# Kernel optimization log

Measured on AMD Instinct MI355X. Metric: run time of the kernel, lower is better.

Reference implementation:

```python
import jax, jax.numpy as jnp
import numpy as np

B, S, DIM, SECL = 32, 2048, 1024, 16  # dim = 2*hidden_dim


def setup_inputs() -> dict:
    key = jax.random.key(0)
    ks = jax.random.split(key, 10)
    return {
        "dec_hidden": jax.random.normal(ks[0], (B, DIM), jnp.float32),
        "enc_output": jax.random.normal(ks[1], (B, S, DIM), jnp.float32),
        "enc_feature": jax.random.normal(ks[2], (B, S, DIM), jnp.float32),
        "enc_mask": jnp.ones((B, S), jnp.float32),
        "sec_attn": jax.random.uniform(ks[3], (B, SECL), jnp.float32),
        "coverage": jax.random.uniform(ks[4], (B, S), jnp.float32),
        "W_dec": jax.random.normal(ks[5], (DIM, DIM), jnp.float32) * (1.0 / np.sqrt(DIM)),
        "b_dec": jax.random.normal(ks[6], (DIM,), jnp.float32) * 0.01,
        "v": jax.random.normal(ks[7], (DIM,), jnp.float32) * (1.0 / np.sqrt(DIM)),
        "w_cov": jax.random.normal(ks[8], (DIM,), jnp.float32) * 0.1,
    }


def reference(dec_hidden, enc_output, enc_feature, enc_mask, sec_attn, coverage,
              W_dec, b_dec, v, w_cov):
    # dec_feature: [B, dim], broadcast over src_len
    dec_feature = dec_hidden @ W_dec.T + b_dec
    # att_features = enc_feature + dec_feature + coverage * w_cov  -> [B, S, dim]
    att = enc_feature + dec_feature[:, None, :] + coverage[:, :, None] * w_cov[None, None, :]
    # scalar score per position: v . tanh(att)  -> [B, S]
    score = jnp.einsum('bsd,d->bs', jnp.tanh(att), v)
    # NOTE: the original multiplies sec_attn*score into attn_dist but immediately
    # overwrites it with softmax(score)*mask, so sec_attn does not affect outputs.
    attn = jax.nn.softmax(score, axis=1) * enc_mask
    attn = attn / jnp.sum(attn, axis=1, keepdims=True)
    # context = attn @ enc_output  -> [B, dim]
    context = jnp.einsum('bs,bsd->bd', attn, enc_output)
    coverage_new = coverage + attn
    return context, attn, coverage_new
```

## Files before the change

### kernel.cpp

```cpp
#include <hip/hip_runtime.h>

#define BB 32
#define SS 2048
#define DD 1024

typedef float f32x4 __attribute__((ext_vector_type(4)));

#if defined(__has_builtin)
#  if __has_builtin(__builtin_amdgcn_exp2f)
#    define EXP2F(x) __builtin_amdgcn_exp2f(x)
#  endif
#  if __has_builtin(__builtin_amdgcn_rcpf)
#    define RCPF(x) __builtin_amdgcn_rcpf(x)
#  endif
#endif
#ifndef EXP2F
#  define EXP2F(x) exp2f(x)
#endif
#ifndef RCPF
#  define RCPF(x) (1.0f / (x))
#endif

#define LOG2E 1.44269504088896340736f

__device__ __forceinline__ float fast_tanh(float x) {
    x = fminf(fmaxf(x, -20.0f), 20.0f);
    float e = EXP2F(x * (2.0f * LOG2E));
    return (e - 1.0f) * RCPF(e + 1.0f);
}

__device__ __forceinline__ f32x4 ntload4(const float* p) {
    return __builtin_nontemporal_load((const f32x4*)p);
}

__global__ __launch_bounds__(256) void k_decfeat(
    const float* __restrict__ dh, const float* __restrict__ W,
    const float* __restrict__ bd, float* __restrict__ df) {
    int wave = threadIdx.x >> 6, lane = threadIdx.x & 63;
    int i = blockIdx.x * 4 + wave;
    f32x4 w[4];
#pragma unroll
    for (int r = 0; r < 4; ++r)
        w[r] = ntload4(W + (size_t)i * DD + (lane + 64 * r) * 4);
    float bi = bd[i];
    for (int b = 0; b < BB; ++b) {
        const float* drow = dh + (size_t)b * DD;
        float acc = 0.0f;
#pragma unroll
        for (int r = 0; r < 4; ++r) {
            f32x4 d = *(const f32x4*)(drow + (lane + 64 * r) * 4);
            acc += w[r].x * d.x + w[r].y * d.y + w[r].z * d.z + w[r].w * d.w;
        }
#pragma unroll
        for (int off = 32; off; off >>= 1) acc += __shfl_down(acc, off, 64);
        if (lane == 0) df[(size_t)b * DD + i] = acc + bi;
    }
}

__global__ __launch_bounds__(256) void k_score(
    const float* __restrict__ ef, const float* __restrict__ df,
    const float* __restrict__ cov, const float* __restrict__ v,
    const float* __restrict__ wc, float* __restrict__ E) {
    int b  = blockIdx.x >> 8;
    int s0 = (blockIdx.x & 255) * 8;
    int t  = threadIdx.x;
    float4 v4 = ((const float4*)v)[t];
    float4 w4 = ((const float4*)wc)[t];
    float4 d4 = ((const float4*)(df + (size_t)b * DD))[t];
    float part[8];
#pragma unroll
    for (int k = 0; k < 8; ++k) {
        int s = s0 + k;
        float c = cov[b * SS + s];
        f32x4 e4 = ntload4(ef + ((size_t)b * SS + s) * DD + t * 4);
        float t0 = fast_tanh(e4.x + d4.x + c * w4.x);
        float t1 = fast_tanh(e4.y + d4.y + c * w4.y);
        float t2 = fast_tanh(e4.z + d4.z + c * w4.z);
        float t3 = fast_tanh(e4.w + d4.w + c * w4.w);
        part[k] = v4.x * t0 + v4.y * t1 + v4.z * t2 + v4.w * t3;
    }
    __shared__ float red[4][8];
    int lane = t & 63, wave = t >> 6;
#pragma unroll
    for (int k = 0; k < 8; ++k) {
        float p = part[k];
#pragma unroll
        for (int off = 32; off; off >>= 1) p += __shfl_down(p, off, 64);
        if (lane == 0) red[wave][k] = p;
    }
    __syncthreads();
    if (t < 8) {
        float sc = red[0][t] + red[1][t] + red[2][t] + red[3][t];
        E[b * SS + s0 + t] = EXP2F(sc * LOG2E);
    }
}

__global__ __launch_bounds__(256) void k_sumexp(
    const float* __restrict__ E, const float* __restrict__ mask,
    float* __restrict__ inv) {
    int b = blockIdx.x, t = threadIdx.x;
    int lane = t & 63, wave = t >> 6;
    float sum = 0.0f;
#pragma unroll
    for (int k = 0; k < 8; ++k) {
        int s = t + 256 * k;
        sum += E[b * SS + s] * mask[b * SS + s];
    }
#pragma unroll
    for (int off = 32; off; off >>= 1) sum += __shfl_down(sum, off, 64);
    __shared__ float red[4];
    if (lane == 0) red[wave] = sum;
    __syncthreads();
    if (t == 0) inv[b] = 1.0f / (red[0] + red[1] + red[2] + red[3]);
}

__global__ __launch_bounds__(256) void k_ctx_part(
    const float* __restrict__ eo, const float* __restrict__ E,
    const float* __restrict__ mask, const float* __restrict__ cov,
    const float* __restrict__ inv, float* __restrict__ attn,
    float* __restrict__ covnew, float* __restrict__ part) {
    int b = blockIdx.x >> 5, ch = blockIdx.x & 31;
    int t = threadIdx.x;
    int s0 = ch * 64;
    __shared__ float als[64];
    if (t < 64) {
        int s = s0 + t;
        float a = E[b * SS + s] * mask[b * SS + s] * inv[b];
        attn[b * SS + s] = a;
        covnew[b * SS + s] = cov[b * SS + s] + a;
        als[t] = a;
    }
    __syncthreads();
    const float* base = eo + ((size_t)b * SS + s0) * DD;
    f32x4 acc = {0.f, 0.f, 0.f, 0.f};
#pragma unroll 8
    for (int k = 0; k < 64; ++k) {
        f32x4 e4 = ntload4(base + (size_t)k * DD + t * 4);
        acc += als[k] * e4;
    }
    ((f32x4*)part)[((size_t)b * 32 + ch) * 256 + t] = acc;
}

__global__ __launch_bounds__(256) void k_ctx_reduce(
    const float* __restrict__ part, float* __restrict__ ctx) {
    int b = blockIdx.x >> 3, dt = blockIdx.x & 7;
    int t = threadIdx.x;
    int slot = t & 31, grp = t >> 5;
    int f4 = dt * 32 + slot;
    const f32x4* p = (const f32x4*)part;
    f32x4 acc = {0.f, 0.f, 0.f, 0.f};
#pragma unroll
    for (int j = 0; j < 4; ++j) {
        int ch = grp + 8 * j;
        acc += p[((size_t)b * 32 + ch) * 256 + f4];
    }
    __shared__ f32x4 red[8][32];
    red[grp][slot] = acc;
    __syncthreads();
    if (t < 32) {
        f32x4 s = red[0][t];
#pragma unroll
        for (int g = 1; g < 8; ++g) s += red[g][t];
        ((f32x4*)ctx)[(size_t)b * 256 + dt * 32 + t] = s;
    }
}

extern "C" void kernel_launch(void* const* d_in, const int* in_sizes, int n_in,
                              void* d_out, int out_size, void* d_ws, size_t ws_size,
                              hipStream_t stream) {
    const float* dec_hidden  = (const float*)d_in[0];
    const float* enc_output  = (const float*)d_in[1];
    const float* enc_feature = (const float*)d_in[2];
    const float* enc_mask    = (const float*)d_in[3];
    const float* coverage    = (const float*)d_in[5];
    const float* W_dec       = (const float*)d_in[6];
    const float* b_dec       = (const float*)d_in[7];
    const float* v           = (const float*)d_in[8];
    const float* w_cov       = (const float*)d_in[9];

    float* ctx    = (float*)d_out;
    float* attn   = (float*)d_out + BB * DD;
    float* covnew = (float*)d_out + BB * DD + BB * SS;

    char* ws = (char*)d_ws;
    float* df   = (float*)(ws);
    float* E    = (float*)(ws + 131072);
    float* inv  = (float*)(ws + 131072 + 262144);
    float* part = (float*)(ws + 131072 + 262144 + 1024);

    k_decfeat   <<<256,   256, 0, stream>>>(dec_hidden, W_dec, b_dec, df);
    k_score     <<<8192,  256, 0, stream>>>(enc_feature, df, coverage, v, w_cov, E);
    k_sumexp    <<<BB,    256, 0, stream>>>(E, enc_mask, inv);
    k_ctx_part  <<<BB*32, 256, 0, stream>>>(enc_output, E, enc_mask, coverage, inv,
                                            attn, covnew, part);
    k_ctx_reduce<<<BB*8,  256, 0, stream>>>(part, ctx);
}
```

Measured before the change: 105.4 us.

## Fold softmax denominator into score kernel via atomics; restructure dec-feature GEMV

Removes the separate sum-of-exponentials kernel: each score block sums its eight masked exponentials and atomically adds them into a per-batch accumulator, which is zeroed by the dec-feature kernel and inverted in the context kernel. The dec-feature GEMV is reorganised so each thread handles one batch row and a 128-element slice for four outputs, with a shared-memory reduction. This saves one launch and one pass over E, at the cost of 8192 atomics and floating-point summation order that varies from run to run.

Result: slower. 165.7 us (+57.2%).

```diff
diff --git a/kernel.cpp b/kernel.cpp
--- a/kernel.cpp
+++ b/kernel.cpp
@@ -35,32 +35,43 @@
 
 __global__ __launch_bounds__(256) void k_decfeat(
     const float* __restrict__ dh, const float* __restrict__ W,
-    const float* __restrict__ bd, float* __restrict__ df) {
-    int wave = threadIdx.x >> 6, lane = threadIdx.x & 63;
-    int i = blockIdx.x * 4 + wave;
-    f32x4 w[4];
+    const float* __restrict__ bd, float* __restrict__ df,
+    float* __restrict__ sum) {
+    if (blockIdx.x == 0 && threadIdx.x < BB) sum[threadIdx.x] = 0.0f;
+    int i0 = blockIdx.x * 4;
+    int t = threadIdx.x;
+    int b = t & 31, e = t >> 5;
+    const f32x4* dhp = (const f32x4*)(dh + (size_t)b * DD + e * 128);
+    f32x4 acc0 = {0,0,0,0}, acc1 = {0,0,0,0}, acc2 = {0,0,0,0}, acc3 = {0,0,0,0};
+    const float* wbase = W + (size_t)i0 * DD + e * 128;
+#pragma unroll 8
+    for (int j = 0; j < 32; ++j) {
+        f32x4 d = dhp[j];
+        acc0 += (*(const f32x4*)(wbase + 0 * DD + j * 4)) * d;
+        acc1 += (*(const f32x4*)(wbase + 1 * DD + j * 4)) * d;
+        acc2 += (*(const f32x4*)(wbase + 2 * DD + j * 4)) * d;
+        acc3 += (*(const f32x4*)(wbase + 3 * DD + j * 4)) * d;
+    }
+    __shared__ float red[32][8][4];
+    red[b][e][0] = acc0.x + acc0.y + acc0.z + acc0.w;
+    red[b][e][1] = acc1.x + acc1.y + acc1.z + acc1.w;
+    red[b][e][2] = acc2.x + acc2.y + acc2.z + acc2.w;
+    red[b][e][3] = acc3.x + acc3.y + acc3.z + acc3.w;
+    __syncthreads();
+    if (t < 128) {
+        int b2 = t & 31, ic = t >> 5;
+        float s = 0.0f;
 #pragma unroll
-    for (int r = 0; r < 4; ++r)
-        w[r] = ntload4(W + (size_t)i * DD + (lane + 64 * r) * 4);
-    float bi = bd[i];
-    for (int b = 0; b < BB; ++b) {
-        const float* drow = dh + (size_t)b * DD;
-        float acc = 0.0f;
-#pragma unroll
-        for (int r = 0; r < 4; ++r) {
-            f32x4 d = *(const f32x4*)(drow + (lane + 64 * r) * 4);
-            acc += w[r].x * d.x + w[r].y * d.y + w[r].z * d.z + w[r].w * d.w;
-        }
-#pragma unroll
-        for (int off = 32; off; off >>= 1) acc += __shfl_down(acc, off, 64);
-        if (lane == 0) df[(size_t)b * DD + i] = acc + bi;
+        for (int k = 0; k < 8; ++k) s += red[b2][k][ic];
+        df[(size_t)b2 * DD + i0 + ic] = s + bd[i0 + ic];
     }
 }
 
 __global__ __launch_bounds__(256) void k_score(
     const float* __restrict__ ef, const float* __restrict__ df,
     const float* __restrict__ cov, const float* __restrict__ v,
-    const float* __restrict__ wc, float* __restrict__ E) {
+    const float* __restrict__ wc, const float* __restrict__ mask,
+    float* __restrict__ E, float* __restrict__ sum) {
     int b  = blockIdx.x >> 8;
     int s0 = (blockIdx.x & 255) * 8;
     int t  = threadIdx.x;
@@ -80,6 +91,7 @@
         part[k] = v4.x * t0 + v4.y * t1 + v4.z * t2 + v4.w * t3;
     }
     __shared__ float red[4][8];
+    __shared__ float em8[8];
     int lane = t & 63, wave = t >> 6;
 #pragma unroll
     for (int k = 0; k < 8; ++k) {
@@ -91,41 +103,31 @@
     __syncthreads();
     if (t < 8) {
         float sc = red[0][t] + red[1][t] + red[2][t] + red[3][t];
-        E[b * SS + s0 + t] = EXP2F(sc * LOG2E);
+        float ee = EXP2F(sc * LOG2E);
+        E[b * SS + s0 + t] = ee;
+        em8[t] = ee * mask[b * SS + s0 + t];
     }
-}
-
-__global__ __launch_bounds__(256) void k_sumexp(
-    const float* __restrict__ E, const float* __restrict__ mask,
-    float* __restrict__ inv) {
-    int b = blockIdx.x, t = threadIdx.x;
-    int lane = t & 63, wave = t >> 6;
-    float sum = 0.0f;
-#pragma unroll
-    for (int k = 0; k < 8; ++k) {
-        int s = t + 256 * k;
-        sum += E[b * SS + s] * mask[b * SS + s];
+    __syncthreads();
+    if (t == 0) {
+        float s = em8[0] + em8[1] + em8[2] + em8[3]
+                + em8[4] + em8[5] + em8[6] + em8[7];
+        atomicAdd(sum + b, s);
     }
-#pragma unroll
-    for (int off = 32; off; off >>= 1) sum += __shfl_down(sum, off, 64);
-    __shared__ float red[4];
-    if (lane == 0) red[wave] = sum;
-    __syncthreads();
-    if (t == 0) inv[b] = 1.0f / (red[0] + red[1] + red[2] + red[3]);
 }
 
 __global__ __launch_bounds__(256) void k_ctx_part(
     const float* __restrict__ eo, const float* __restrict__ E,
     const float* __restrict__ mask, const float* __restrict__ cov,
-    const float* __restrict__ inv, float* __restrict__ attn,
+    const float* __restrict__ sum, float* __restrict__ attn,
     float* __restrict__ covnew, float* __restrict__ part) {
     int b = blockIdx.x >> 5, ch = blockIdx.x & 31;
     int t = threadIdx.x;
     int s0 = ch * 64;
+    float invb = RCPF(sum[b]);
     __shared__ float als[64];
     if (t < 64) {
         int s = s0 + t;
-        float a = E[b * SS + s] * mask[b * SS + s] * inv[b];
+        float a = E[b * SS + s] * mask[b * SS + s] * invb;
         attn[b * SS + s] = a;
         covnew[b * SS + s] = cov[b * SS + s] + a;
         als[t] = a;
@@ -185,13 +187,13 @@
     char* ws = (char*)d_ws;
     float* df   = (float*)(ws);
     float* E    = (float*)(ws + 131072);
-    float* inv  = (float*)(ws + 131072 + 262144);
-    float* part = (float*)(ws + 131072 + 262144 + 1024);
+    float* sum  = (float*)(ws + 393216);
+    float* part = (float*)(ws + 394240);
 
-    k_decfeat   <<<256,   256, 0, stream>>>(dec_hidden, W_dec, b_dec, df);
-    k_score     <<<8192,  256, 0, stream>>>(enc_feature, df, coverage, v, w_cov, E);
-    k_sumexp    <<<BB,    256, 0, stream>>>(E, enc_mask, inv);
-    k_ctx_part  <<<BB*32, 256, 0, stream>>>(enc_output, E, enc_mask, coverage, inv,
+    k_decfeat   <<<256,   256, 0, stream>>>(dec_hidden, W_dec, b_dec, df, sum);
+    k_score     <<<8192,  256, 0, stream>>>(enc_feature, df, coverage, v, w_cov,
+                                            enc_mask, E, sum);
+    k_ctx_part  <<<BB*32, 256, 0, stream>>>(enc_output, E, enc_mask, coverage, sum,
                                             attn, covnew, part);
     k_ctx_reduce<<<BB*8,  256, 0, stream>>>(part, ctx);
 }
```

## Fuse softmax sum into context kernel and reduce context with atomics

Applied to the files above, without the earlier changes.

The separate sum-of-exp kernel is folded into the context kernel: each of the 32 blocks per batch recomputes the full 2048-element normalizer redundantly. The partial-context buffer and its reduce kernel are replaced by float atomicAdd into a ctx buffer that the decoder-feature kernel zeroes. The decoder GEMV is re-parallelized to one wave per output element across 8192 blocks, which drops W register reuse across the batch. Together these cut two launches and the partial round trip, at the cost of redundant sums, atomic contention and nondeterministic summation order.

Result: faster. 100.5 us (-4.7%).

```diff
diff --git a/kernel.cpp b/kernel.cpp
--- a/kernel.cpp
+++ b/kernel.cpp
@@ -35,26 +35,28 @@
 
 __global__ __launch_bounds__(256) void k_decfeat(
     const float* __restrict__ dh, const float* __restrict__ W,
-    const float* __restrict__ bd, float* __restrict__ df) {
-    int wave = threadIdx.x >> 6, lane = threadIdx.x & 63;
-    int i = blockIdx.x * 4 + wave;
-    f32x4 w[4];
+    const float* __restrict__ bd, float* __restrict__ df,
+    float* __restrict__ ctx) {
+    if (blockIdx.x < BB) {
+        f32x4 z = {0.f, 0.f, 0.f, 0.f};
+        ((f32x4*)ctx)[blockIdx.x * 256 + threadIdx.x] = z;
+    }
+    int wave = threadIdx.x >> 6;
+    int lane = threadIdx.x & 63;
+    int o = blockIdx.x * 4 + wave;
+    int b = o >> 10, i = o & 1023;
+    const float4* wrow = (const float4*)(W + (size_t)i * DD);
+    const float4* drow = (const float4*)(dh + (size_t)b * DD);
+    float acc = 0.0f;
 #pragma unroll
-    for (int r = 0; r < 4; ++r)
-        w[r] = ntload4(W + (size_t)i * DD + (lane + 64 * r) * 4);
-    float bi = bd[i];
-    for (int b = 0; b < BB; ++b) {
-        const float* drow = dh + (size_t)b * DD;
-        float acc = 0.0f;
+    for (int r = 0; r < 4; ++r) {
+        float4 w4 = wrow[lane + 64 * r];
+        float4 d4 = drow[lane + 64 * r];
+        acc += w4.x * d4.x + w4.y * d4.y + w4.z * d4.z + w4.w * d4.w;
+    }
 #pragma unroll
-        for (int r = 0; r < 4; ++r) {
-            f32x4 d = *(const f32x4*)(drow + (lane + 64 * r) * 4);
-            acc += w[r].x * d.x + w[r].y * d.y + w[r].z * d.z + w[r].w * d.w;
-        }
-#pragma unroll
-        for (int off = 32; off; off >>= 1) acc += __shfl_down(acc, off, 64);
-        if (lane == 0) df[(size_t)b * DD + i] = acc + bi;
-    }
+    for (int off = 32; off; off >>= 1) acc += __shfl_down(acc, off, 64);
+    if (lane == 0) df[o] = acc + bd[i];
 }
 
 __global__ __launch_bounds__(256) void k_score(
@@ -95,10 +97,13 @@
     }
 }
 
-__global__ __launch_bounds__(256) void k_sumexp(
-    const float* __restrict__ E, const float* __restrict__ mask,
-    float* __restrict__ inv) {
-    int b = blockIdx.x, t = threadIdx.x;
+__global__ __launch_bounds__(256) void k_ctx_part(
+    const float* __restrict__ eo, const float* __restrict__ E,
+    const float* __restrict__ mask, const float* __restrict__ cov,
+    float* __restrict__ attn, float* __restrict__ covnew,
+    float* __restrict__ ctx) {
+    int b = blockIdx.x >> 5, ch = blockIdx.x & 31;
+    int t = threadIdx.x;
     int lane = t & 63, wave = t >> 6;
     float sum = 0.0f;
 #pragma unroll
@@ -109,23 +114,16 @@
 #pragma unroll
     for (int off = 32; off; off >>= 1) sum += __shfl_down(sum, off, 64);
     __shared__ float red[4];
+    __shared__ float invs;
     if (lane == 0) red[wave] = sum;
     __syncthreads();
-    if (t == 0) inv[b] = 1.0f / (red[0] + red[1] + red[2] + red[3]);
-}
-
-__global__ __launch_bounds__(256) void k_ctx_part(
-    const float* __restrict__ eo, const float* __restrict__ E,
-    const float* __restrict__ mask, const float* __restrict__ cov,
-    const float* __restrict__ inv, float* __restrict__ attn,
-    float* __restrict__ covnew, float* __restrict__ part) {
-    int b = blockIdx.x >> 5, ch = blockIdx.x & 31;
-    int t = threadIdx.x;
+    if (t == 0) invs = RCPF(red[0] + red[1] + red[2] + red[3]);
+    __syncthreads();
     int s0 = ch * 64;
     __shared__ float als[64];
     if (t < 64) {
         int s = s0 + t;
-        float a = E[b * SS + s] * mask[b * SS + s] * inv[b];
+        float a = E[b * SS + s] * mask[b * SS + s] * invs;
         attn[b * SS + s] = a;
         covnew[b * SS + s] = cov[b * SS + s] + a;
         als[t] = a;
@@ -138,31 +136,11 @@
         f32x4 e4 = ntload4(base + (size_t)k * DD + t * 4);
         acc += als[k] * e4;
     }
-    ((f32x4*)part)[((size_t)b * 32 + ch) * 256 + t] = acc;
-}
-
-__global__ __launch_bounds__(256) void k_ctx_reduce(
-    const float* __restrict__ part, float* __restrict__ ctx) {
-    int b = blockIdx.x >> 3, dt = blockIdx.x & 7;
-    int t = threadIdx.x;
-    int slot = t & 31, grp = t >> 5;
-    int f4 = dt * 32 + slot;
-    const f32x4* p = (const f32x4*)part;
-    f32x4 acc = {0.f, 0.f, 0.f, 0.f};
-#pragma unroll
-    for (int j = 0; j < 4; ++j) {
-        int ch = grp + 8 * j;
-        acc += p[((size_t)b * 32 + ch) * 256 + f4];
-    }
-    __shared__ f32x4 red[8][32];
-    red[grp][slot] = acc;
-    __syncthreads();
-    if (t < 32) {
-        f32x4 s = red[0][t];
-#pragma unroll
-        for (int g = 1; g < 8; ++g) s += red[g][t];
-        ((f32x4*)ctx)[(size_t)b * 256 + dt * 32 + t] = s;
-    }
+    float* cp = ctx + (size_t)b * DD + t * 4;
+    atomicAdd(cp + 0, acc.x);
+    atomicAdd(cp + 1, acc.y);
+    atomicAdd(cp + 2, acc.z);
+    atomicAdd(cp + 3, acc.w);
 }
 
 extern "C" void kernel_launch(void* const* d_in, const int* in_sizes, int n_in,
@@ -183,15 +161,11 @@
     float* covnew = (float*)d_out + BB * DD + BB * SS;
 
     char* ws = (char*)d_ws;
-    float* df   = (float*)(ws);
-    float* E    = (float*)(ws + 131072);
-    float* inv  = (float*)(ws + 131072 + 262144);
-    float* part = (float*)(ws + 131072 + 262144 + 1024);
+    float* df = (float*)(ws);
+    float* E  = (float*)(ws + 131072);
 
-    k_decfeat   <<<256,   256, 0, stream>>>(dec_hidden, W_dec, b_dec, df);
-    k_score     <<<8192,  256, 0, stream>>>(enc_feature, df, coverage, v, w_cov, E);
-    k_sumexp    <<<BB,    256, 0, stream>>>(E, enc_mask, inv);
-    k_ctx_part  <<<BB*32, 256, 0, stream>>>(enc_output, E, enc_mask, coverage, inv,
-                                            attn, covnew, part);
-    k_ctx_reduce<<<BB*8,  256, 0, stream>>>(part, ctx);
+    k_decfeat  <<<8192,  256, 0, stream>>>(dec_hidden, W_dec, b_dec, df, ctx);
+    k_score    <<<8192,  256, 0, stream>>>(enc_feature, df, coverage, v, w_cov, E);
+    k_ctx_part <<<BB*32, 256, 0, stream>>>(enc_output, E, enc_mask, coverage,
+                                           attn, covnew, ctx);
 }
```
